# Performance work log

Hardware: AMD Instinct MI355X
Metric: run time of the kernel (lower is better)

Reference implementation:

```python
import jax, jax.numpy as jnp
import numpy as np
import math

B, DIM, P = 8192, 4096, 64
PI = math.pi
LN_EPS = 1e-5


def setup_inputs() -> dict:
    key = jax.random.key(0)
    ks = jax.random.split(key, 8)
    s_enc = 1.0 / math.sqrt(DIM)
    return {
        "x": jax.random.normal(ks[0], (B, DIM), dtype=jnp.float32),
        "Wk": jax.random.normal(ks[1], (P, DIM), dtype=jnp.float32) * s_enc,
        "bk": jnp.zeros((P,), dtype=jnp.float32),
        "Wq": jax.random.normal(ks[2], (P, DIM), dtype=jnp.float32) * s_enc,
        "bq": jnp.zeros((P,), dtype=jnp.float32),
        "Wv": jax.random.normal(ks[3], (DIM, DIM), dtype=jnp.float32) * s_enc,
        "bv": jnp.zeros((DIM,), dtype=jnp.float32),
        "ln_g": jnp.ones((DIM,), dtype=jnp.float32),
        "ln_b": jnp.zeros((DIM,), dtype=jnp.float32),
        "Wo": jax.random.normal(ks[4], (DIM, DIM), dtype=jnp.float32) * s_enc,
        "bo": jnp.zeros((DIM,), dtype=jnp.float32),
    }


def reference(x, Wk, bk, Wq, bq, Wv, bv, ln_g, ln_b, Wo, bo):
    # phases in [-pi, pi]
    key_phase = jnp.tanh(x @ Wk.T + bk) * PI    # [B, P]
    query_phase = jnp.tanh(x @ Wq.T + bq) * PI  # [B, P]
    # key_phasor * conj(query_phasor) = exp(i*(kp-qp)); its real part:
    phase_alignment = jnp.cos(key_phase - query_phase)  # [B, P]
    align_sum = jnp.sum(phase_alignment, axis=-1, keepdims=True)  # [B, 1]
    # V is real, so sum_p(retrieved).real = V * sum_p cos(kp-qp) exactly
    V = x @ Wv.T + bv  # [B, DIM]
    resonance = align_sum / P
    resonance_gain = jax.nn.softplus(resonance + 0.5)  # [B, 1]
    summed = V * align_sum  # [B, DIM]
    output = summed * resonance_gain / P
    # to_out: LayerNorm then Linear
    mu = jnp.mean(output, axis=-1, keepdims=True)
    var = jnp.mean(jnp.square(output - mu), axis=-1, keepdims=True)
    normed = (output - mu) * jax.lax.rsqrt(var + LN_EPS) * ln_g + ln_b
    return x + normed @ Wo.T + bo
```

## Files before the change

kernel.cpp:

```cpp
#include <hip/hip_runtime.h>
#include <hip/hip_bf16.h>
#include <math.h>
#include <stdint.h>

#define PI_F 3.14159265358979323846f

typedef __hip_bfloat16 bf16;
typedef __attribute__((ext_vector_type(8))) short short8;
typedef __attribute__((ext_vector_type(4))) float floatx4;

static constexpr int DIM = 4096;

__device__ __forceinline__ unsigned short f2bf_bits(float f) {
    __hip_bfloat16 h = __float2bfloat16(f);
    return __builtin_bit_cast(unsigned short, h);
}
__device__ __forceinline__ float bf2f_bits(unsigned short u) {
    return __builtin_bit_cast(float, ((unsigned int)u) << 16);
}
__device__ __forceinline__ void load_lds16(const void* gsrc, void* lds) {
    __builtin_amdgcn_global_load_lds(
        (__attribute__((address_space(1))) void*)gsrc,
        (__attribute__((address_space(3))) void*)lds,
        16, 0, 0);
}

__global__ __launch_bounds__(256)
void cast_f32_bf16(const float* __restrict__ src, unsigned short* __restrict__ dst, int n4) {
    int i = blockIdx.x * 256 + threadIdx.x;
    if (i < n4) {
        float4 v = ((const float4*)src)[i];
        ushort4 o;
        o.x = f2bf_bits(v.x); o.y = f2bf_bits(v.y);
        o.z = f2bf_bits(v.z); o.w = f2bf_bits(v.w);
        ((ushort4*)dst)[i] = o;
    }
}

__global__ __launch_bounds__(256)
void transpose_wkq(const float* __restrict__ Wk, const float* __restrict__ Wq,
                   float* __restrict__ Wt) {
    int idx = blockIdx.x * 256 + threadIdx.x;
    int k = idx >> 7, p = idx & 127;
    float v = (p < 64) ? Wk[(size_t)p * DIM + k] : Wq[(size_t)(p - 64) * DIM + k];
    Wt[idx] = v;
}

__global__ __launch_bounds__(256)
void phase_partial(const float* __restrict__ x, const float* __restrict__ Wt,
                   float* __restrict__ part)
{
    const int tid = threadIdx.x;
    const int rg  = tid >> 5;
    const int cg  = tid & 31;
    const size_t row0 = (size_t)blockIdx.x * 32;
    const int s   = blockIdx.y;
    const int kbeg = s * 512, kend = kbeg + 512;

    float acc[4][4] = {};
    const float* xp = x + (row0 + (size_t)rg * 4) * DIM;

    for (int k = kbeg; k < kend; k += 4) {
        const float4 w0 = *(const float4*)(Wt + (size_t)(k + 0) * 128 + cg * 4);
        const float4 w1 = *(const float4*)(Wt + (size_t)(k + 1) * 128 + cg * 4);
        const float4 w2 = *(const float4*)(Wt + (size_t)(k + 2) * 128 + cg * 4);
        const float4 w3 = *(const float4*)(Wt + (size_t)(k + 3) * 128 + cg * 4);
        #pragma unroll
        for (int r = 0; r < 4; ++r) {
            const float4 xv = *(const float4*)(xp + (size_t)r * DIM + k);
            acc[r][0] += xv.x * w0.x + xv.y * w1.x + xv.z * w2.x + xv.w * w3.x;
            acc[r][1] += xv.x * w0.y + xv.y * w1.y + xv.z * w2.y + xv.w * w3.y;
            acc[r][2] += xv.x * w0.z + xv.y * w1.z + xv.z * w2.z + xv.w * w3.z;
            acc[r][3] += xv.x * w0.w + xv.y * w1.w + xv.z * w2.w + xv.w * w3.w;
        }
    }

    #pragma unroll
    for (int r = 0; r < 4; ++r) {
        float4 st;
        st.x = acc[r][0]; st.y = acc[r][1]; st.z = acc[r][2]; st.w = acc[r][3];
        *(float4*)(part + ((size_t)s * 8192 + row0 + rg * 4 + r) * 128 + cg * 4) = st;
    }
}

__global__ __launch_bounds__(256)
void phase_finalize(const float* __restrict__ part, const float* __restrict__ bk,
                    const float* __restrict__ bq, float* __restrict__ scale)
{
    const int tid  = threadIdx.x;
    const int lane = tid & 63;
    const size_t row = (size_t)blockIdx.x * 4 + (tid >> 6);
    float sk = 0.f, sq = 0.f;
    #pragma unroll
    for (int s = 0; s < 8; ++s) {
        const float* pr = part + ((size_t)s * 8192 + row) * 128;
        sk += pr[lane];
        sq += pr[64 + lane];
    }
    const float kp = PI_F * tanhf(sk + bk[lane]);
    const float qp = PI_F * tanhf(sq + bq[lane]);
    float c = cosf(kp - qp);
    #pragma unroll
    for (int off = 32; off; off >>= 1) c += __shfl_down(c, off, 64);
    if (lane == 0) {
        const float a = c;
        const float gsp = log1pf(expf(a * (1.f / 64.f) + 0.5f));
        scale[row] = a * gsp * (1.f / 64.f);
    }
}

#define VM6 asm volatile("s_waitcnt vmcnt(6)" ::: "memory")
#define VM4 asm volatile("s_waitcnt vmcnt(4)" ::: "memory")
#define VM2 asm volatile("s_waitcnt vmcnt(2)" ::: "memory")
#define VM0 asm volatile("s_waitcnt vmcnt(0)" ::: "memory")
#define VMNONE

#define STAGE_A(buf, t, R0) load_lds16(A  + gAoff + (size_t)(R0) * 4096 + (size_t)(t) * 64, \
                                       smem + (buf) * 32768 + ((R0) + (wv << 3)) * 64)
#define STAGE_B(buf, t, R0) load_lds16(Bm + gBoff + (size_t)(R0) * 4096 + (size_t)(t) * 64, \
                                       smem + (buf) * 32768 + 16384 + ((R0) + (wv << 3)) * 64)

#define MM(MH, i, j, af, bfv) \
    acc[(MH) * 4 + (i)][(j)] = __builtin_amdgcn_mfma_f32_16x16x32_bf16((af), (bfv), acc[(MH) * 4 + (i)][(j)], 0, 0, 0)

#define PHASE(BUF, MH, KS, STAGES, WAITS) do {                                   \
    const int swzc = ((((KS) * 4) + q) ^ (m16 & 7)) * 8;                         \
    const bf16* pa = smem + (BUF) * 32768 + arow0 + (MH) * 4096 + swzc;          \
    const bf16* pb = smem + (BUF) * 32768 + 16384 + brow0 + swzc;                \
    short8 a0 = *(const short8*)(pa);                                            \
    short8 a1 = *(const short8*)(pa + 1024);                                     \
    short8 a2 = *(const short8*)(pa + 2048);                                     \
    short8 a3 = *(const short8*)(pa + 3072);                                     \
    short8 b0 = *(const short8*)(pb);                                            \
    short8 b1 = *(const short8*)(pb + 1024);                                     \
    short8 b2 = *(const short8*)(pb + 2048);                                     \
    short8 b3 = *(const short8*)(pb + 3072);                                     \
    STAGES;                                                                      \
    __builtin_amdgcn_s_barrier();                                                \
    __builtin_amdgcn_s_setprio(1);                                               \
    MM(MH,0,0,a0,b0); MM(MH,0,1,a0,b1); MM(MH,0,2,a0,b2); MM(MH,0,3,a0,b3);      \
    MM(MH,1,0,a1,b0); MM(MH,1,1,a1,b1); MM(MH,1,2,a1,b2); MM(MH,1,3,a1,b3);      \
    MM(MH,2,0,a2,b0); MM(MH,2,1,a2,b1); MM(MH,2,2,a2,b2); MM(MH,2,3,a2,b3);      \
    MM(MH,3,0,a3,b0); MM(MH,3,1,a3,b1); MM(MH,3,2,a3,b2); MM(MH,3,3,a3,b3);      \
    __builtin_amdgcn_s_setprio(0);                                               \
    WAITS;                                                                       \
    __builtin_amdgcn_s_barrier();                                                \
} while (0)

#define WINDOW(W, BUF, DOB, DOA1, DOA0, W1, W3)                                  \
    do {                                                                         \
        PHASE(BUF, 0, 0,                                                         \
              if (DOB) { STAGE_B((BUF) ^ 1, (W) + 1, 0); STAGE_B((BUF) ^ 1, (W) + 1, 64); },  \
              VMNONE);                                                           \
        PHASE(BUF, 0, 1,                                                         \
              if (DOB) { STAGE_B((BUF) ^ 1, (W) + 1, 128); STAGE_B((BUF) ^ 1, (W) + 1, 192); }, \
              W1);                                                               \
        PHASE(BUF, 1, 0,                                                         \
              if (DOA1) { STAGE_A((BUF) ^ 1, (W) + 1, 64); STAGE_A((BUF) ^ 1, (W) + 1, 192); }, \
              VMNONE);                                                           \
        PHASE(BUF, 1, 1,                                                         \
              if (DOA0) { STAGE_A((BUF), (W) + 2, 0); STAGE_A((BUF), (W) + 2, 128); },          \
              W3);                                                               \
    } while (0)

template <int MODE>
__global__ __launch_bounds__(512, 2)
void gemm256(const bf16* __restrict__ A, const bf16* __restrict__ Bm,
             const float* __restrict__ bias, const float* __restrict__ scale,
             const float* __restrict__ xres, bf16* __restrict__ outBf,
             float* __restrict__ outF)
{
    __shared__ __align__(16) bf16 smem[2 * 2 * 256 * 64];

    const int tid  = threadIdx.x;
    const int lane = tid & 63;
    const int wv   = tid >> 6;
    const int wm   = wv >> 2;
    const int wn   = wv & 3;
    const int q    = lane >> 4;
    const int m16  = lane & 15;

    const int lid = blockIdx.x;
    const int swz = (lid & 7) * 64 + (lid >> 3);
    const size_t bm = (size_t)(swz & 31) * 256;
    const size_t bn = (size_t)(swz >> 5) * 256;

    const int srow = (wv << 3) + (lane >> 3);
    const int schk = (lane & 7) ^ (lane >> 3);
    const size_t gAoff = (bm + srow) * 4096 + schk * 8;
    const size_t gBoff = (bn + srow) * 4096 + schk * 8;

    const int arow0 = (wm * 128 + m16) * 64;
    const int brow0 = (wn * 64 + m16) * 64;

    floatx4 acc[8][4] = {};

    STAGE_A(0, 0, 0);  STAGE_A(0, 0, 64);  STAGE_A(0, 0, 128); STAGE_A(0, 0, 192);
    STAGE_B(0, 0, 0);  STAGE_B(0, 0, 64);  STAGE_B(0, 0, 128); STAGE_B(0, 0, 192);
    STAGE_A(1, 1, 0);  STAGE_A(1, 1, 128);
    VM2;
    __builtin_amdgcn_s_barrier();

    for (int w = 0; w < 62; w += 2) {
        WINDOW(w,     0, 1, 1, 1, VM6, VM4);
        WINDOW(w + 1, 1, 1, 1, 1, VM6, VM4);
    }
    WINDOW(62, 0, 1, 1, 0, VM6, VM2);
    WINDOW(63, 1, 0, 0, 0, VM0, VMNONE);

    #pragma unroll
    for (int ii = 0; ii < 8; ++ii) {
        const int mh = ii >> 2, i = ii & 3;
        #pragma unroll
        for (int j = 0; j < 4; ++j) {
            const size_t col = bn + wn * 64 + j * 16 + m16;
            const float bvv = bias[col];
            #pragma unroll
            for (int r = 0; r < 4; ++r) {
                const size_t row = bm + wm * 128 + mh * 64 + i * 16 + q * 4 + r;
                float v = acc[ii][j][r] + bvv;
                if (MODE == 1) {
                    v *= scale[row];
                    outBf[row * 4096 + col] = __float2bfloat16(v);
                } else {
                    v += xres[row * 4096 + col];
                    outF[row * 4096 + col] = v;
                }
            }
        }
    }
}

__global__ __launch_bounds__(256)
void ln_kernel(bf16* __restrict__ o, const float* __restrict__ g, const float* __restrict__ b)
{
    const size_t row = blockIdx.x;
    unsigned short* p = (unsigned short*)(o + row * DIM);
    const int tid = threadIdx.x;
    float s = 0.f, s2 = 0.f;
    float vals[16];
    #pragma unroll
    for (int c = 0; c < 4; ++c) {
        ushort4 u = ((const ushort4*)p)[tid + c * 256];
        float v0 = bf2f_bits(u.x), v1 = bf2f_bits(u.y);
        float v2 = bf2f_bits(u.z), v3 = bf2f_bits(u.w);
        vals[c * 4 + 0] = v0; vals[c * 4 + 1] = v1;
        vals[c * 4 + 2] = v2; vals[c * 4 + 3] = v3;
        s  += v0 + v1 + v2 + v3;
        s2 += v0 * v0 + v1 * v1 + v2 * v2 + v3 * v3;
    }
    #pragma unroll
    for (int off = 32; off; off >>= 1) {
        s  += __shfl_down(s, off, 64);
        s2 += __shfl_down(s2, off, 64);
    }
    __shared__ float red[2][4];
    const int wv = tid >> 6, ln = tid & 63;
    if (ln == 0) { red[0][wv] = s; red[1][wv] = s2; }
    __syncthreads();
    const float ts  = red[0][0] + red[0][1] + red[0][2] + red[0][3];
    const float ts2 = red[1][0] + red[1][1] + red[1][2] + red[1][3];
    const float mean = ts * (1.f / 4096.f);
    const float var  = ts2 * (1.f / 4096.f) - mean * mean;
    const float rstd = rsqrtf(var + 1e-5f);
    #pragma unroll
    for (int c = 0; c < 4; ++c) {
        const int idx = (tid + c * 256) * 4;
        ushort4 u;
        u.x = f2bf_bits((vals[c * 4 + 0] - mean) * rstd * g[idx + 0] + b[idx + 0]);
        u.y = f2bf_bits((vals[c * 4 + 1] - mean) * rstd * g[idx + 1] + b[idx + 1]);
        u.z = f2bf_bits((vals[c * 4 + 2] - mean) * rstd * g[idx + 2] + b[idx + 2]);
        u.w = f2bf_bits((vals[c * 4 + 3] - mean) * rstd * g[idx + 3] + b[idx + 3]);
        ((ushort4*)p)[tid + c * 256] = u;
    }
}

extern "C" void kernel_launch(void* const* d_in, const int* in_sizes, int n_in,
                              void* d_out, int out_size, void* d_ws, size_t ws_size,
                              hipStream_t stream)
{
    const float* x   = (const float*)d_in[0];
    const float* Wk  = (const float*)d_in[1];
    const float* bk  = (const float*)d_in[2];
    const float* Wq  = (const float*)d_in[3];
    const float* bq  = (const float*)d_in[4];
    const float* Wv  = (const float*)d_in[5];
    const float* bv  = (const float*)d_in[6];
    const float* lng = (const float*)d_in[7];
    const float* lnb = (const float*)d_in[8];
    const float* Wo  = (const float*)d_in[9];
    const float* bo  = (const float*)d_in[10];

    char* ws = (char*)d_ws;
    bf16*  x_bf  = (bf16*)(ws);
    bf16*  Wv_bf = (bf16*)(ws + 67108864);
    bf16*  Wo_bf = (bf16*)(ws + 100663296);
    float* Wt    = (float*)(ws + 134217728);
    float* scl   = (float*)(ws + 136314880);
    bf16*  nbuf  = (bf16*)(ws + 136347648);
    float* part  = (float*)nbuf;

    cast_f32_bf16<<<8388608 / 256, 256, 0, stream>>>(x,  (unsigned short*)x_bf,  8388608);
    cast_f32_bf16<<<4194304 / 256, 256, 0, stream>>>(Wv, (unsigned short*)Wv_bf, 4194304);
    cast_f32_bf16<<<4194304 / 256, 256, 0, stream>>>(Wo, (unsigned short*)Wo_bf, 4194304);
    transpose_wkq<<<2048, 256, 0, stream>>>(Wk, Wq, Wt);
    phase_partial<<<dim3(256, 8), 256, 0, stream>>>(x, Wt, part);
    phase_finalize<<<2048, 256, 0, stream>>>(part, bk, bq, scl);
    gemm256<1><<<512, 512, 0, stream>>>(x_bf, Wv_bf, bv, scl, nullptr, nbuf, nullptr);
    ln_kernel<<<8192, 256, 0, stream>>>(nbuf, lng, lnb);
    gemm256<2><<<512, 512, 0, stream>>>(nbuf, Wo_bf, bo, nullptr, x, nullptr, (float*)d_out);
}
```

Measured before the change: 1.120 ms.

## Compute phase projections with split bf16 hi/lo MFMA instead of fp32 FMA

Replaces the scalar fp32 phase projection (x @ [Wk;Wq]^T) with a bf16 MFMA kernel that uses a hi/lo split (three MFMAs per tile) to keep near-fp32 accuracy. The x cast now also emits a low-residual bf16 buffer, which aliases the Wv bf16 region, so the Wv/Wo casts are moved after the phase kernels. The aim is to remove the CUDA-core-bound FMA loop, at the cost of writing an extra x residual buffer and tripling the MFMA work for this small GEMM.

```diff
diff --git a/kernel.cpp b/kernel.cpp
--- a/kernel.cpp
+++ b/kernel.cpp
@@ -38,48 +38,118 @@
 }
 
 __global__ __launch_bounds__(256)
-void transpose_wkq(const float* __restrict__ Wk, const float* __restrict__ Wq,
-                   float* __restrict__ Wt) {
-    int idx = blockIdx.x * 256 + threadIdx.x;
-    int k = idx >> 7, p = idx & 127;
-    float v = (p < 64) ? Wk[(size_t)p * DIM + k] : Wq[(size_t)(p - 64) * DIM + k];
-    Wt[idx] = v;
-}
-
-__global__ __launch_bounds__(256)
-void phase_partial(const float* __restrict__ x, const float* __restrict__ Wt,
-                   float* __restrict__ part)
-{
-    const int tid = threadIdx.x;
-    const int rg  = tid >> 5;
-    const int cg  = tid & 31;
-    const size_t row0 = (size_t)blockIdx.x * 32;
-    const int s   = blockIdx.y;
-    const int kbeg = s * 512, kend = kbeg + 512;
-
-    float acc[4][4] = {};
-    const float* xp = x + (row0 + (size_t)rg * 4) * DIM;
-
-    for (int k = kbeg; k < kend; k += 4) {
-        const float4 w0 = *(const float4*)(Wt + (size_t)(k + 0) * 128 + cg * 4);
-        const float4 w1 = *(const float4*)(Wt + (size_t)(k + 1) * 128 + cg * 4);
-        const float4 w2 = *(const float4*)(Wt + (size_t)(k + 2) * 128 + cg * 4);
-        const float4 w3 = *(const float4*)(Wt + (size_t)(k + 3) * 128 + cg * 4);
+void cast_f32_bf16_hilo(const float* __restrict__ src, unsigned short* __restrict__ hi,
+                        unsigned short* __restrict__ lo, int n4) {
+    int i = blockIdx.x * 256 + threadIdx.x;
+    if (i < n4) {
+        float4 v = ((const float4*)src)[i];
+        ushort4 h, l;
+        h.x = f2bf_bits(v.x); l.x = f2bf_bits(v.x - bf2f_bits(h.x));
+        h.y = f2bf_bits(v.y); l.y = f2bf_bits(v.y - bf2f_bits(h.y));
+        h.z = f2bf_bits(v.z); l.z = f2bf_bits(v.z - bf2f_bits(h.z));
+        h.w = f2bf_bits(v.w); l.w = f2bf_bits(v.w - bf2f_bits(h.w));
+        ((ushort4*)hi)[i] = h;
+        ((ushort4*)lo)[i] = l;
+    }
+}
+
+__global__ __launch_bounds__(256)
+void cast_wkq_hilo(const float* __restrict__ Wk, const float* __restrict__ Wq,
+                   unsigned short* __restrict__ hi, unsigned short* __restrict__ lo) {
+    int i = blockIdx.x * 256 + threadIdx.x;
+    const int n = i >> 10;
+    const int c4 = i & 1023;
+    const float* src = (n < 64) ? (Wk + (size_t)n * DIM) : (Wq + (size_t)(n - 64) * DIM);
+    float4 v = ((const float4*)src)[c4];
+    ushort4 h, l;
+    h.x = f2bf_bits(v.x); l.x = f2bf_bits(v.x - bf2f_bits(h.x));
+    h.y = f2bf_bits(v.y); l.y = f2bf_bits(v.y - bf2f_bits(h.y));
+    h.z = f2bf_bits(v.z); l.z = f2bf_bits(v.z - bf2f_bits(h.z));
+    h.w = f2bf_bits(v.w); l.w = f2bf_bits(v.w - bf2f_bits(h.w));
+    ((ushort4*)hi)[i] = h;
+    ((ushort4*)lo)[i] = l;
+}
+
+__global__ __launch_bounds__(256)
+void phase_mfma(const bf16* __restrict__ xh, const bf16* __restrict__ xl,
+                const bf16* __restrict__ wh, const bf16* __restrict__ wl,
+                float* __restrict__ part)
+{
+    __shared__ __align__(16) bf16 sm[12288];
+    const int tid  = threadIdx.x;
+    const int lane = tid & 63;
+    const int wv   = tid >> 6;
+    const int wm   = wv >> 1;
+    const int wn   = wv & 1;
+    const int q    = lane >> 4;
+    const int m16  = lane & 15;
+
+    const size_t bm = (size_t)blockIdx.x * 64;
+    const int s    = blockIdx.y;
+    const int kbeg = s * 512;
+
+    const int sr = lane >> 2;
+    const int sc = (lane & 3) ^ (sr & 3) ^ ((sr >> 2) & 3);
+    const size_t gA  = (bm + (size_t)wv * 16 + sr) * 4096 + kbeg + sc * 8;
+    const size_t gB0 = ((size_t)wv * 32 + sr) * 4096 + kbeg + sc * 8;
+    const size_t gB1 = gB0 + (size_t)16 * 4096;
+
+    bf16* lAh  = sm + wv * 512;
+    bf16* lAl  = sm + 2048 + wv * 512;
+    bf16* lBh0 = sm + 4096 + wv * 1024;
+    bf16* lBh1 = sm + 4096 + wv * 1024 + 512;
+    bf16* lBl0 = sm + 8192 + wv * 1024;
+    bf16* lBl1 = sm + 8192 + wv * 1024 + 512;
+
+    const int sl    = ((q ^ ((m16 & 3) ^ ((m16 >> 2) & 3))) * 8);
+    const int aoff0 = (wm * 32 + m16) * 32 + sl;
+    const int aoff1 = aoff0 + 16 * 32;
+
+    floatx4 acc[2][4] = {};
+
+    for (int t = 0; t < 16; ++t) {
+        const size_t ko = (size_t)t * 32;
+        load_lds16(xh + gA  + ko, lAh);
+        load_lds16(xl + gA  + ko, lAl);
+        load_lds16(wh + gB0 + ko, lBh0);
+        load_lds16(wh + gB1 + ko, lBh1);
+        load_lds16(wl + gB0 + ko, lBl0);
+        load_lds16(wl + gB1 + ko, lBl1);
+        __syncthreads();
+        short8 ah0 = *(const short8*)(sm + aoff0);
+        short8 ah1 = *(const short8*)(sm + aoff1);
+        short8 al0 = *(const short8*)(sm + 2048 + aoff0);
+        short8 al1 = *(const short8*)(sm + 2048 + aoff1);
+        short8 bh[4], bl[4];
         #pragma unroll
-        for (int r = 0; r < 4; ++r) {
-            const float4 xv = *(const float4*)(xp + (size_t)r * DIM + k);
-            acc[r][0] += xv.x * w0.x + xv.y * w1.x + xv.z * w2.x + xv.w * w3.x;
-            acc[r][1] += xv.x * w0.y + xv.y * w1.y + xv.z * w2.y + xv.w * w3.y;
-            acc[r][2] += xv.x * w0.z + xv.y * w1.z + xv.z * w2.z + xv.w * w3.z;
-            acc[r][3] += xv.x * w0.w + xv.y * w1.w + xv.z * w2.w + xv.w * w3.w;
+        for (int j = 0; j < 4; ++j) {
+            const int boff = (wn * 64 + j * 16 + m16) * 32 + sl;
+            bh[j] = *(const short8*)(sm + 4096 + boff);
+            bl[j] = *(const short8*)(sm + 8192 + boff);
         }
-    }
-
-    #pragma unroll
-    for (int r = 0; r < 4; ++r) {
-        float4 st;
-        st.x = acc[r][0]; st.y = acc[r][1]; st.z = acc[r][2]; st.w = acc[r][3];
-        *(float4*)(part + ((size_t)s * 8192 + row0 + rg * 4 + r) * 128 + cg * 4) = st;
+        #pragma unroll
+        for (int j = 0; j < 4; ++j) {
+            acc[0][j] = __builtin_amdgcn_mfma_f32_16x16x32_bf16(ah0, bh[j], acc[0][j], 0, 0, 0);
+            acc[0][j] = __builtin_amdgcn_mfma_f32_16x16x32_bf16(ah0, bl[j], acc[0][j], 0, 0, 0);
+            acc[0][j] = __builtin_amdgcn_mfma_f32_16x16x32_bf16(al0, bh[j], acc[0][j], 0, 0, 0);
+            acc[1][j] = __builtin_amdgcn_mfma_f32_16x16x32_bf16(ah1, bh[j], acc[1][j], 0, 0, 0);
+            acc[1][j] = __builtin_amdgcn_mfma_f32_16x16x32_bf16(ah1, bl[j], acc[1][j], 0, 0, 0);
+            acc[1][j] = __builtin_amdgcn_mfma_f32_16x16x32_bf16(al1, bh[j], acc[1][j], 0, 0, 0);
+        }
+        __syncthreads();
+    }
+
+    #pragma unroll
+    for (int i = 0; i < 2; ++i) {
+        #pragma unroll
+        for (int j = 0; j < 4; ++j) {
+            const int col = wn * 64 + j * 16 + m16;
+            #pragma unroll
+            for (int r = 0; r < 4; ++r) {
+                const size_t row = bm + wm * 32 + i * 16 + q * 4 + r;
+                part[((size_t)s * 8192 + row) * 128 + col] = acc[i][j][r];
+            }
+        }
     }
 }
 
@@ -292,20 +362,24 @@
     const float* bo  = (const float*)d_in[10];
 
     char* ws = (char*)d_ws;
-    bf16*  x_bf  = (bf16*)(ws);
-    bf16*  Wv_bf = (bf16*)(ws + 67108864);
-    bf16*  Wo_bf = (bf16*)(ws + 100663296);
-    float* Wt    = (float*)(ws + 134217728);
-    float* scl   = (float*)(ws + 136314880);
-    bf16*  nbuf  = (bf16*)(ws + 136347648);
-    float* part  = (float*)nbuf;
-
-    cast_f32_bf16<<<8388608 / 256, 256, 0, stream>>>(x,  (unsigned short*)x_bf,  8388608);
+    bf16*  x_bf   = (bf16*)(ws);
+    bf16*  x_lo   = (bf16*)(ws + 67108864);
+    bf16*  Wv_bf  = (bf16*)(ws + 67108864);
+    bf16*  Wo_bf  = (bf16*)(ws + 100663296);
+    bf16*  Wkq_hi = (bf16*)(ws + 134217728);
+    bf16*  Wkq_lo = (bf16*)(ws + 135266304);
+    float* scl    = (float*)(ws + 136314880);
+    bf16*  nbuf   = (bf16*)(ws + 136347648);
+    float* part   = (float*)nbuf;
+
+    cast_f32_bf16_hilo<<<8388608 / 256, 256, 0, stream>>>(x, (unsigned short*)x_bf,
+                                                          (unsigned short*)x_lo, 8388608);
+    cast_wkq_hilo<<<131072 / 256, 256, 0, stream>>>(Wk, Wq, (unsigned short*)Wkq_hi,
+                                                    (unsigned short*)Wkq_lo);
+    phase_mfma<<<dim3(128, 8), 256, 0, stream>>>(x_bf, x_lo, Wkq_hi, Wkq_lo, part);
+    phase_finalize<<<2048, 256, 0, stream>>>(part, bk, bq, scl);
     cast_f32_bf16<<<4194304 / 256, 256, 0, stream>>>(Wv, (unsigned short*)Wv_bf, 4194304);
     cast_f32_bf16<<<4194304 / 256, 256, 0, stream>>>(Wo, (unsigned short*)Wo_bf, 4194304);
-    transpose_wkq<<<2048, 256, 0, stream>>>(Wk, Wq, Wt);
-    phase_partial<<<dim3(256, 8), 256, 0, stream>>>(x, Wt, part);
-    phase_finalize<<<2048, 256, 0, stream>>>(part, bk, bq, scl);
     gemm256<1><<<512, 512, 0, stream>>>(x_bf, Wv_bf, bv, scl, nullptr, nbuf, nullptr);
     ln_kernel<<<8192, 256, 0, stream>>>(nbuf, lng, lnb);
     gemm256<2><<<512, 512, 0, stream>>>(nbuf, Wo_bf, bo, nullptr, x, nullptr, (float*)d_out);
```

Result: faster. 945.2 us (-15.6%).
